# Kernel tuning notes

Hardware: AMD Instinct MI355X
Metric: run time of the kernel (lower is better)

The kernel has to match this reference:

```python
import jax, jax.numpy as jnp
import numpy as np

D_MODEL = 1024
D_FF = 1024
NUM_EXPERTS = 8
TOP_K = 2


def setup_inputs() -> dict:
    key = jax.random.key(0)
    ks = jax.random.split(key, 5)
    s_in = 1.0 / np.sqrt(D_MODEL)
    s_ff = 1.0 / np.sqrt(D_FF)
    return {
        "x": jax.random.normal(ks[0], (4, 2048, D_MODEL), dtype=jnp.float32),
        "gate_w": jax.random.normal(ks[1], (NUM_EXPERTS, D_MODEL), dtype=jnp.float32) * s_in,
        # torch Linear weight layout: [out_features, in_features], stacked over experts
        "w_gate": jax.random.normal(ks[2], (NUM_EXPERTS, D_FF, D_MODEL), dtype=jnp.float32) * s_in,
        "w_up": jax.random.normal(ks[3], (NUM_EXPERTS, D_FF, D_MODEL), dtype=jnp.float32) * s_in,
        "w_down": jax.random.normal(ks[4], (NUM_EXPERTS, D_MODEL, D_FF), dtype=jnp.float32) * s_ff,
    }


def reference(x, gate_w, w_gate, w_up, w_down):
    B, S, D = x.shape
    T = B * S
    E = gate_w.shape[0]
    xt = x.reshape(T, D)

    # Router
    logits = xt @ gate_w.T                      # [T, E]
    probs = jax.nn.softmax(logits, axis=-1)
    top_v, top_i = jax.lax.top_k(probs, TOP_K)  # [T, K]
    top_v = top_v / jnp.sum(top_v, axis=-1, keepdims=True)

    tokens_per_expert = jnp.sum(jax.nn.one_hot(top_i, E, dtype=jnp.float32), axis=(0, 1))  # [E]
    f = tokens_per_expert / jnp.sum(tokens_per_expert)
    P = jnp.mean(probs, axis=0)
    aux_loss = E * jnp.sum(f * P)

    # Combine weights: per-token weight for each expert (sum over top-k slots)
    combine = jnp.zeros((T, E), dtype=x.dtype).at[jnp.arange(T)[:, None], top_i].add(top_v)  # [T, E]

    # Dense per-expert SwiGLU (equivalent math to masked gather/scatter loop)
    g = jnp.einsum('td,efd->etf', xt, w_gate)   # [E, T, F]
    u = jnp.einsum('td,efd->etf', xt, w_up)     # [E, T, F]
    act = jax.nn.silu(g) * u
    eo = jnp.einsum('etf,edf->etd', act, w_down)  # [E, T, D]

    out = jnp.einsum('te,etd->td', combine, eo).reshape(B, S, D)
    return out, aux_loss, tokens_per_expert
```

## Files before the change

### kernel.cpp

```cpp
#include <hip/hip_runtime.h>


#define T_TOK   8192
#define DM      1024
#define DFF     1024
#define NE      8
#define TOTS    (2 * T_TOK)
#define R1_BLK  2048
#define CVT_BLK 2048

typedef __attribute__((ext_vector_type(8))) short bf16x8;
typedef __attribute__((ext_vector_type(4))) float f32x4;

#define ASYNC16(gp, lp) __builtin_amdgcn_global_load_lds( \
    (const __attribute__((address_space(1))) unsigned int*)(gp), \
    (__attribute__((address_space(3))) unsigned int*)(lp), 16, 0, 0)

__device__ __forceinline__ unsigned short f2bf(float f) {
    union { float f; unsigned u; } c; c.f = f;
    unsigned r = c.u + 0x7fffu + ((c.u >> 16) & 1u);
    return (unsigned short)(r >> 16);
}
__device__ __forceinline__ float bf2f(unsigned short h) {
    union { unsigned u; float f; } c; c.u = ((unsigned)h) << 16;
    return c.f;
}

__global__ __launch_bounds__(256) void pre_kernel(
    const float* __restrict__ x, const float* __restrict__ gate_w,
    const float* __restrict__ s0, const float* __restrict__ s1, const float* __restrict__ s2,
    unsigned short* __restrict__ d0, unsigned short* __restrict__ d1, unsigned short* __restrict__ d2,
    unsigned short* __restrict__ xb,
    int* __restrict__ topi, float2* __restrict__ topw, float* __restrict__ psum_part)
{
    int tid = threadIdx.x;
    int sub = blockIdx.x >> 1;

    if (blockIdx.x & 1) {
        int base = sub * 256 + tid;
        #pragma unroll
        for (int it = 0; it < 12; ++it) {
            int idx = base + it * (CVT_BLK * 256);
            int seg = idx >> 21;
            int off = (idx & ((1 << 21) - 1)) * 4;
            const float* s = (seg == 0) ? s0 : (seg == 1) ? s1 : s2;
            unsigned short* d = (seg == 0) ? d0 : (seg == 1) ? d1 : d2;
            float4 v = *(const float4*)(s + off);
            ushort4 o;
            o.x = f2bf(v.x); o.y = f2bf(v.y); o.z = f2bf(v.z); o.w = f2bf(v.w);
            *(ushort4*)(d + off) = o;
        }
        return;
    }

    __shared__ float gw[NE * DM];
    __shared__ float blk_psum[NE];

    for (int i = tid; i < NE * DM; i += 256) gw[i] = gate_w[i];
    if (tid < NE) blk_psum[tid] = 0.f;
    __syncthreads();

    int wv = tid >> 6, lane = tid & 63;
    int t = sub * 4 + wv;

    float acc[NE];
    #pragma unroll
    for (int e = 0; e < NE; ++e) acc[e] = 0.f;
    const float* xr = x + (size_t)t * DM;
    unsigned short* xbr = xb + (size_t)t * DM;
    #pragma unroll 4
    for (int i = 0; i < DM / 64; ++i) {
        float xv = xr[i * 64 + lane];
        xbr[i * 64 + lane] = f2bf(xv);
        #pragma unroll
        for (int e = 0; e < NE; ++e)
            acc[e] += xv * gw[e * DM + i * 64 + lane];
    }
    #pragma unroll
    for (int e = 0; e < NE; ++e) {
        float v = acc[e];
        #pragma unroll
        for (int s = 32; s > 0; s >>= 1) v += __shfl_xor(v, s, 64);
        acc[e] = v;
    }
    if (lane == 0) {
        float mx = acc[0];
        #pragma unroll
        for (int e = 1; e < NE; ++e) mx = fmaxf(mx, acc[e]);
        float p[NE], sum = 0.f;
        #pragma unroll
        for (int e = 0; e < NE; ++e) { p[e] = expf(acc[e] - mx); sum += p[e]; }
        float inv = 1.f / sum;
        #pragma unroll
        for (int e = 0; e < NE; ++e) { p[e] *= inv; atomicAdd(&blk_psum[e], p[e]); }
        int i1 = 0; float v1 = p[0];
        #pragma unroll
        for (int e = 1; e < NE; ++e) if (p[e] > v1) { v1 = p[e]; i1 = e; }
        int i2 = -1; float v2 = -1.f;
        #pragma unroll
        for (int e = 0; e < NE; ++e) { if (e == i1) continue; if (p[e] > v2) { v2 = p[e]; i2 = e; } }
        float winv = 1.f / (v1 + v2);
        topi[t] = i1 | (i2 << 8);
        topw[t] = make_float2(v1 * winv, v2 * winv);
    }
    __syncthreads();
    if (tid < NE) psum_part[sub * NE + tid] = blk_psum[tid];
}

__global__ __launch_bounds__(1024) void scatfin_kernel(
    const int* __restrict__ topi, const float* __restrict__ psum_part,
    int* __restrict__ elist, int2* __restrict__ cidx,
    int* __restrict__ ecnt, int* __restrict__ ebaseg, float* __restrict__ out_tail)
{
    __shared__ int lcnt[NE], run[NE], cb[NE], ebase[NE];
    __shared__ float parts[NE];
    __shared__ float red[1024];
    int tid = threadIdx.x;

    if (tid < NE) run[tid] = 0;
    __syncthreads();
    #pragma unroll
    for (int ch = 0; ch < T_TOK / 1024; ++ch) {
        int tt = ch * 1024 + tid;
        int pk = topi[tt];
        int e1 = pk & 0xff, e2 = (pk >> 8) & 0xff;
        if (tid < NE) lcnt[tid] = 0;
        __syncthreads();
        int p1 = atomicAdd(&lcnt[e1], 1);
        int p2 = atomicAdd(&lcnt[e2], 1);
        __syncthreads();
        if (tid < NE) { cb[tid] = run[tid]; run[tid] += lcnt[tid]; }
        __syncthreads();
        cidx[tt] = make_int2(cb[e1] + p1, cb[e2] + p2);
    }
    __syncthreads();
    if (tid == 0) {
        int s = 0;
        for (int e = 0; e < NE; ++e) { ebase[e] = s; s += run[e]; }
    }
    __syncthreads();
    #pragma unroll
    for (int ch = 0; ch < T_TOK / 1024; ++ch) {
        int tt = ch * 1024 + tid;
        int pk = topi[tt];
        int e1 = pk & 0xff, e2 = (pk >> 8) & 0xff;
        int2 pp = cidx[tt];
        int r1 = ebase[e1] + pp.x, r2 = ebase[e2] + pp.y;
        elist[r1] = tt;
        elist[r2] = tt;
        cidx[tt] = make_int2(r1, r2);
    }
    if (tid < NE) { ecnt[tid] = run[tid]; ebaseg[tid] = ebase[tid]; }

    int e = tid & 7, b0 = tid >> 3;
    float s = 0.f;
    for (int b = b0; b < R1_BLK; b += 128) s += psum_part[b * NE + e];
    red[tid] = s;
    __syncthreads();
    if (tid < NE) {
        float tot = 0.f;
        #pragma unroll
        for (int j = 0; j < 128; ++j) tot += red[tid + NE * j];
        float P = tot / (float)T_TOK;
        float f = (float)run[tid] / (float)(2 * T_TOK);
        parts[tid] = f * P;
        out_tail[1 + tid] = (float)run[tid];
    }
    __syncthreads();
    if (tid == 0) {
        float s2 = 0.f;
        for (int i = 0; i < NE; ++i) s2 += parts[i];
        out_tail[0] = (float)NE * s2;
    }
}

__global__ __launch_bounds__(256) void gemm1_kernel(
    const unsigned short* __restrict__ xb,
    const unsigned short* __restrict__ wgb,
    const unsigned short* __restrict__ wub,
    const int* __restrict__ elist, const int* __restrict__ ecnt,
    const int* __restrict__ ebaseg,
    unsigned short* __restrict__ Hbuf)
{
    int e = blockIdx.z, mt = blockIdx.y, ft = blockIdx.x;
    int ne = ecnt[e];
    if (mt * 128 >= ne) return;
    int base = ebaseg[e];

    __shared__ unsigned short As[128 * 64];
    __shared__ unsigned short Gs[64 * 64];
    __shared__ unsigned short Us[64 * 64];
    __shared__ int tok[128];

    int tid = threadIdx.x;
    if (tid < 128) {
        int slot = base + mt * 128 + tid;
        tok[tid] = elist[min(slot, TOTS - 1)];
    }
    __syncthreads();

    int wave = tid >> 6, lane = tid & 63;
    int quad = lane >> 4, col = lane & 15;
    int cr = tid >> 3;
    int cl = ((tid & 7) ^ (cr & 7)) * 8;

    const size_t woff = (size_t)e * (size_t)DFF * DM;
    const unsigned short* ap[4];
    #pragma unroll
    for (int j = 0; j < 4; ++j) ap[j] = xb + (size_t)tok[j * 32 + cr] * DM + cl;
    const unsigned short* gp[2];
    const unsigned short* up[2];
    #pragma unroll
    for (int j = 0; j < 2; ++j) {
        gp[j] = wgb + woff + (size_t)(ft * 64 + j * 32 + cr) * DM + cl;
        up[j] = wub + woff + (size_t)(ft * 64 + j * 32 + cr) * DM + cl;
    }
    unsigned short* lA = As + wave * 512;
    unsigned short* lG = Gs + wave * 512;
    unsigned short* lU = Us + wave * 512;

    f32x4 accG[2][4], accU[2][4];
    #pragma unroll
    for (int i = 0; i < 2; ++i)
        #pragma unroll
        for (int n = 0; n < 4; ++n) { accG[i][n] = (f32x4){0,0,0,0}; accU[i][n] = (f32x4){0,0,0,0}; }

    for (int k0 = 0; k0 < DM; k0 += 64) {
        __syncthreads();
        #pragma unroll
        for (int j = 0; j < 4; ++j) ASYNC16(ap[j] + k0, lA + j * 2048);
        #pragma unroll
        for (int j = 0; j < 2; ++j) {
            ASYNC16(gp[j] + k0, lG + j * 2048);
            ASYNC16(up[j] + k0, lU + j * 2048);
        }
        __syncthreads();
        #pragma unroll
        for (int ksoff = 0; ksoff < 8; ksoff += 4) {
            bf16x8 a[2], g[4], u[4];
            #pragma unroll
            for (int i = 0; i < 2; ++i) {
                int m = wave * 32 + i * 16 + col;
                a[i] = *(const bf16x8*)&As[m * 64 + ((quad + ksoff) ^ (m & 7)) * 8];
            }
            #pragma unroll
            for (int n = 0; n < 4; ++n) {
                int nb = n * 16 + col;
                int off = nb * 64 + ((quad + ksoff) ^ (nb & 7)) * 8;
                g[n] = *(const bf16x8*)&Gs[off];
                u[n] = *(const bf16x8*)&Us[off];
            }
            #pragma unroll
            for (int i = 0; i < 2; ++i)
                #pragma unroll
                for (int n = 0; n < 4; ++n) {
                    accG[i][n] = __builtin_amdgcn_mfma_f32_16x16x32_bf16(a[i], g[n], accG[i][n], 0, 0, 0);
                    accU[i][n] = __builtin_amdgcn_mfma_f32_16x16x32_bf16(a[i], u[n], accU[i][n], 0, 0, 0);
                }
        }
    }
    #pragma unroll
    for (int i = 0; i < 2; ++i) {
        #pragma unroll
        for (int r = 0; r < 4; ++r) {
            int pos = mt * 128 + wave * 32 + i * 16 + quad * 4 + r;
            if (pos >= ne) continue;
            unsigned short* hr = Hbuf + (size_t)(base + pos) * DFF + ft * 64 + col;
            #pragma unroll
            for (int n = 0; n < 4; ++n) {
                float gg = accG[i][n][r], uu = accU[i][n][r];
                float h = (gg / (1.f + expf(-gg))) * uu;
                hr[n * 16] = f2bf(h);
            }
        }
    }
}

__global__ __launch_bounds__(256) void gemm2_kernel(
    const unsigned short* __restrict__ Hbuf,
    const unsigned short* __restrict__ wdb,
    const int* __restrict__ ecnt, const int* __restrict__ ebaseg,
    unsigned short* __restrict__ eo)
{
    int e = blockIdx.z, mt = blockIdx.y, dt = blockIdx.x;
    int ne = ecnt[e];
    if (mt * 128 >= ne) return;
    int base = ebaseg[e];

    __shared__ unsigned short As[128 * 64];
    __shared__ unsigned short Bs[128 * 64];

    int tid = threadIdx.x;
    int wave = tid >> 6, lane = tid & 63;
    int quad = lane >> 4, col = lane & 15;
    int wr = (wave >> 1) * 64, wc = (wave & 1) * 64;
    int cr = tid >> 3;
    int cl = ((tid & 7) ^ (cr & 7)) * 8;

    const size_t woff = (size_t)e * (size_t)DM * DFF;
    const unsigned short* ap[4];
    const unsigned short* bp[4];
    #pragma unroll
    for (int j = 0; j < 4; ++j) {
        int hrow = min(base + mt * 128 + j * 32 + cr, TOTS - 1);
        ap[j] = Hbuf + (size_t)hrow * DFF + cl;
        bp[j] = wdb + woff + (size_t)(dt * 128 + j * 32 + cr) * DFF + cl;
    }
    unsigned short* lA = As + wave * 512;
    unsigned short* lB = Bs + wave * 512;

    f32x4 acc[4][4];
    #pragma unroll
    for (int i = 0; i < 4; ++i)
        #pragma unroll
        for (int n = 0; n < 4; ++n) acc[i][n] = (f32x4){0,0,0,0};

    for (int k0 = 0; k0 < DFF; k0 += 64) {
        __syncthreads();
        #pragma unroll
        for (int j = 0; j < 4; ++j) {
            ASYNC16(ap[j] + k0, lA + j * 2048);
            ASYNC16(bp[j] + k0, lB + j * 2048);
        }
        __syncthreads();
        #pragma unroll
        for (int ksoff = 0; ksoff < 8; ksoff += 4) {
            bf16x8 a[4], b[4];
            #pragma unroll
            for (int i = 0; i < 4; ++i) {
                int m = wr + i * 16 + col;
                a[i] = *(const bf16x8*)&As[m * 64 + ((quad + ksoff) ^ (m & 7)) * 8];
            }
            #pragma unroll
            for (int n = 0; n < 4; ++n) {
                int nb = wc + n * 16 + col;
                b[n] = *(const bf16x8*)&Bs[nb * 64 + ((quad + ksoff) ^ (nb & 7)) * 8];
            }
            #pragma unroll
            for (int i = 0; i < 4; ++i)
                #pragma unroll
                for (int n = 0; n < 4; ++n)
                    acc[i][n] = __builtin_amdgcn_mfma_f32_16x16x32_bf16(a[i], b[n], acc[i][n], 0, 0, 0);
        }
    }
    #pragma unroll
    for (int i = 0; i < 4; ++i) {
        #pragma unroll
        for (int r = 0; r < 4; ++r) {
            int pos = mt * 128 + wr + i * 16 + quad * 4 + r;
            if (pos >= ne) continue;
            unsigned short* er = eo + (size_t)(base + pos) * DM + dt * 128 + wc + col;
            #pragma unroll
            for (int n = 0; n < 4; ++n)
                er[n * 16] = f2bf(acc[i][n][r]);
        }
    }
}

__global__ __launch_bounds__(256) void combine_kernel(
    const unsigned short* __restrict__ eo, const float2* __restrict__ topw,
    const int2* __restrict__ cidx, float* __restrict__ out)
{
    int idx = blockIdx.x * 256 + threadIdx.x;
    int t = idx >> 7;
    int c = (idx & 127) << 3;
    float2 w = topw[t];
    int2 rr = cidx[t];
    const unsigned short* p0 = eo + (size_t)rr.x * DM + c;
    const unsigned short* p1 = eo + (size_t)rr.y * DM + c;
    ushort4 a0 = *(const ushort4*)p0;
    ushort4 a1 = *(const ushort4*)(p0 + 4);
    ushort4 b0 = *(const ushort4*)p1;
    ushort4 b1 = *(const ushort4*)(p1 + 4);
    float* orow = out + (size_t)t * DM + c;
    float4 o0, o1;
    o0.x = w.x * bf2f(a0.x) + w.y * bf2f(b0.x);
    o0.y = w.x * bf2f(a0.y) + w.y * bf2f(b0.y);
    o0.z = w.x * bf2f(a0.z) + w.y * bf2f(b0.z);
    o0.w = w.x * bf2f(a0.w) + w.y * bf2f(b0.w);
    o1.x = w.x * bf2f(a1.x) + w.y * bf2f(b1.x);
    o1.y = w.x * bf2f(a1.y) + w.y * bf2f(b1.y);
    o1.z = w.x * bf2f(a1.z) + w.y * bf2f(b1.z);
    o1.w = w.x * bf2f(a1.w) + w.y * bf2f(b1.w);
    *(float4*)orow = o0;
    *(float4*)(orow + 4) = o1;
}

extern "C" void kernel_launch(void* const* d_in, const int* in_sizes, int n_in,
                              void* d_out, int out_size, void* d_ws, size_t ws_size,
                              hipStream_t stream) {
    const float* x      = (const float*)d_in[0];
    const float* gate_w = (const float*)d_in[1];
    const float* w_gate = (const float*)d_in[2];
    const float* w_up   = (const float*)d_in[3];
    const float* w_down = (const float*)d_in[4];
    float* out = (float*)d_out;

    char* p = (char*)d_ws;
    unsigned short* xb   = (unsigned short*)p; p += (size_t)T_TOK * DM * 2;
    unsigned short* wgb  = (unsigned short*)p; p += (size_t)NE * DFF * DM * 2;
    unsigned short* wub  = (unsigned short*)p; p += (size_t)NE * DFF * DM * 2;
    unsigned short* wdb  = (unsigned short*)p; p += (size_t)NE * DM * DFF * 2;
    unsigned short* Hbuf = (unsigned short*)p; p += (size_t)TOTS * DFF * 2;
    int*   elist = (int*)p;   p += (size_t)TOTS * 4;
    int*   ecnt  = (int*)p;   p += NE * 4;
    int*   ebaseg= (int*)p;   p += NE * 4;
    int*   topi  = (int*)p;   p += (size_t)T_TOK * 4;
    float2* topw = (float2*)p; p += (size_t)T_TOK * 8;
    int2*  cidx  = (int2*)p;  p += (size_t)T_TOK * 8;
    float* psum_part = (float*)p; p += (size_t)R1_BLK * NE * 4;
    unsigned short* eo = wgb;

    pre_kernel<<<R1_BLK + CVT_BLK, 256, 0, stream>>>(
        x, gate_w, w_gate, w_up, w_down, wgb, wub, wdb,
        xb, topi, topw, psum_part);
    scatfin_kernel<<<1, 1024, 0, stream>>>(topi, psum_part, elist, cidx, ecnt, ebaseg,
                                           out + (size_t)T_TOK * DM);
    gemm1_kernel<<<dim3(DFF / 64, TOTS / 128, NE), 256, 0, stream>>>(
        xb, wgb, wub, elist, ecnt, ebaseg, Hbuf);
    gemm2_kernel<<<dim3(DM / 128, TOTS / 128, NE), 256, 0, stream>>>(
        Hbuf, wdb, ecnt, ebaseg, eo);
    combine_kernel<<<T_TOK * DM / 8 / 256, 256, 0, stream>>>(eo, topw, cidx, out);
}
```

Baseline: 340.0 us.

## Rewrite expert GEMMs with 256x256 tiles, double-buffered LDS and interleaved async loads

Both grouped expert GEMMs move to 512-thread blocks with 256-row by 256-column output tiles. LDS is double-buffered so the next K slice loads through async global-to-LDS copies while MFMAs run on the current one, with explicit barriers, vmcnt waits and setprio around the MFMA bursts. The larger tiles raise data reuse per block and the pipeline is meant to hide load latency. In exchange each block uses 128KB of LDS, which limits occupancy, the grid has fewer blocks so load balance across experts gets coarser, and the hand-placed waitcnt/barrier sequencing is fragile.

```diff
diff --git a/kernel.cpp b/kernel.cpp
--- a/kernel.cpp
+++ b/kernel.cpp
@@ -15,6 +15,10 @@
 #define ASYNC16(gp, lp) __builtin_amdgcn_global_load_lds( \
     (const __attribute__((address_space(1))) unsigned int*)(gp), \
     (__attribute__((address_space(3))) unsigned int*)(lp), 16, 0, 0)
+
+#define BAR()   __builtin_amdgcn_s_barrier()
+#define SFENCE() __builtin_amdgcn_sched_barrier(0)
+#define VMCNT2() asm volatile("s_waitcnt vmcnt(2)" ::: "memory")
 
 __device__ __forceinline__ unsigned short f2bf(float f) {
     union { float f; unsigned u; } c; c.f = f;
@@ -174,7 +178,7 @@
     }
 }
 
-__global__ __launch_bounds__(256) void gemm1_kernel(
+__global__ __launch_bounds__(512, 2) void gemm1_kernel(
     const unsigned short* __restrict__ xb,
     const unsigned short* __restrict__ wgb,
     const unsigned short* __restrict__ wub,
@@ -184,88 +188,149 @@
 {
     int e = blockIdx.z, mt = blockIdx.y, ft = blockIdx.x;
     int ne = ecnt[e];
-    if (mt * 128 >= ne) return;
+    if (mt * 256 >= ne) return;
     int base = ebaseg[e];
 
-    __shared__ unsigned short As[128 * 64];
-    __shared__ unsigned short Gs[64 * 64];
-    __shared__ unsigned short Us[64 * 64];
-    __shared__ int tok[128];
+    __shared__ unsigned short As[2][256 * 64];
+    __shared__ unsigned short Bs[2][256 * 64];
+    __shared__ int tok[256];
 
     int tid = threadIdx.x;
-    if (tid < 128) {
-        int slot = base + mt * 128 + tid;
-        tok[tid] = elist[min(slot, TOTS - 1)];
-    }
+    if (tid < 256) tok[tid] = elist[min(base + mt * 256 + tid, TOTS - 1)];
     __syncthreads();
 
     int wave = tid >> 6, lane = tid & 63;
+    int wq = wave >> 1, wn = wave & 1;
     int quad = lane >> 4, col = lane & 15;
     int cr = tid >> 3;
     int cl = ((tid & 7) ^ (cr & 7)) * 8;
 
     const size_t woff = (size_t)e * (size_t)DFF * DM;
     const unsigned short* ap[4];
-    #pragma unroll
-    for (int j = 0; j < 4; ++j) ap[j] = xb + (size_t)tok[j * 32 + cr] * DM + cl;
-    const unsigned short* gp[2];
-    const unsigned short* up[2];
+    const unsigned short* bp[4];
+    #pragma unroll
+    for (int j = 0; j < 4; ++j)
+        ap[j] = xb + (size_t)tok[j * 64 + cr] * DM + cl;
     #pragma unroll
     for (int j = 0; j < 2; ++j) {
-        gp[j] = wgb + woff + (size_t)(ft * 64 + j * 32 + cr) * DM + cl;
-        up[j] = wub + woff + (size_t)(ft * 64 + j * 32 + cr) * DM + cl;
-    }
-    unsigned short* lA = As + wave * 512;
-    unsigned short* lG = Gs + wave * 512;
-    unsigned short* lU = Us + wave * 512;
-
-    f32x4 accG[2][4], accU[2][4];
-    #pragma unroll
-    for (int i = 0; i < 2; ++i)
+        bp[j]     = wgb + woff + (size_t)(ft * 128 + j * 64 + cr) * DM + cl;
+        bp[j + 2] = wub + woff + (size_t)(ft * 128 + j * 64 + cr) * DM + cl;
+    }
+
+    f32x4 accG[4][4], accU[4][4];
+    #pragma unroll
+    for (int i = 0; i < 4; ++i)
         #pragma unroll
         for (int n = 0; n < 4; ++n) { accG[i][n] = (f32x4){0,0,0,0}; accU[i][n] = (f32x4){0,0,0,0}; }
 
-    for (int k0 = 0; k0 < DM; k0 += 64) {
-        __syncthreads();
-        #pragma unroll
-        for (int j = 0; j < 4; ++j) ASYNC16(ap[j] + k0, lA + j * 2048);
-        #pragma unroll
-        for (int j = 0; j < 2; ++j) {
-            ASYNC16(gp[j] + k0, lG + j * 2048);
-            ASYNC16(up[j] + k0, lU + j * 2048);
-        }
-        __syncthreads();
-        #pragma unroll
-        for (int ksoff = 0; ksoff < 8; ksoff += 4) {
-            bf16x8 a[2], g[4], u[4];
-            #pragma unroll
-            for (int i = 0; i < 2; ++i) {
-                int m = wave * 32 + i * 16 + col;
-                a[i] = *(const bf16x8*)&As[m * 64 + ((quad + ksoff) ^ (m & 7)) * 8];
-            }
-            #pragma unroll
-            for (int n = 0; n < 4; ++n) {
-                int nb = n * 16 + col;
-                int off = nb * 64 + ((quad + ksoff) ^ (nb & 7)) * 8;
-                g[n] = *(const bf16x8*)&Gs[off];
-                u[n] = *(const bf16x8*)&Us[off];
-            }
-            #pragma unroll
-            for (int i = 0; i < 2; ++i)
-                #pragma unroll
-                for (int n = 0; n < 4; ++n) {
-                    accG[i][n] = __builtin_amdgcn_mfma_f32_16x16x32_bf16(a[i], g[n], accG[i][n], 0, 0, 0);
-                    accU[i][n] = __builtin_amdgcn_mfma_f32_16x16x32_bf16(a[i], u[n], accU[i][n], 0, 0, 0);
-                }
-        }
-    }
-    #pragma unroll
-    for (int i = 0; i < 2; ++i) {
+    {
+        unsigned short* A0 = &As[0][wave * 512];
+        unsigned short* B0 = &Bs[0][wave * 512];
+        #pragma unroll
+        for (int j = 0; j < 4; ++j) ASYNC16(ap[j], A0 + j * 4096);
+        #pragma unroll
+        for (int j = 0; j < 4; ++j) ASYNC16(bp[j], B0 + j * 4096);
+    }
+    asm volatile("s_waitcnt vmcnt(0)" ::: "memory");
+    BAR(); SFENCE();
+
+    for (int t = 0; t < 16; ++t) {
+        int cur = t & 1;
+        int ks = (t < 15 ? (t + 1) : 15) * 64;
+        unsigned short* An = &As[cur ^ 1][wave * 512];
+        unsigned short* Bn = &Bs[cur ^ 1][wave * 512];
+        const unsigned short* Ac = &As[cur][0];
+        const unsigned short* Bc = &Bs[cur][0];
+
+        bf16x8 a[4], b[4];
+        #pragma unroll
+        for (int i = 0; i < 4; ++i) {
+            int m = wq * 64 + i * 16 + col;
+            a[i] = *(const bf16x8*)&Ac[m * 64 + (quad ^ (m & 7)) * 8];
+        }
+        #pragma unroll
+        for (int n = 0; n < 4; ++n) {
+            int nb = wn * 64 + n * 16 + col;
+            b[n] = *(const bf16x8*)&Bc[nb * 64 + (quad ^ (nb & 7)) * 8];
+        }
+        ASYNC16(ap[0] + ks, An);
+        ASYNC16(ap[1] + ks, An + 4096);
+        VMCNT2();
+        BAR(); SFENCE();
+        __builtin_amdgcn_s_setprio(1);
+        #pragma unroll
+        for (int i = 0; i < 4; ++i)
+            #pragma unroll
+            for (int n = 0; n < 4; ++n)
+                accG[i][n] = __builtin_amdgcn_mfma_f32_16x16x32_bf16(a[i], b[n], accG[i][n], 0, 0, 0);
+        __builtin_amdgcn_s_setprio(0);
+        BAR(); SFENCE();
+
+        #pragma unroll
+        for (int n = 0; n < 4; ++n) {
+            int nb = 128 + wn * 64 + n * 16 + col;
+            b[n] = *(const bf16x8*)&Bc[nb * 64 + (quad ^ (nb & 7)) * 8];
+        }
+        ASYNC16(ap[2] + ks, An + 8192);
+        ASYNC16(ap[3] + ks, An + 12288);
+        BAR(); SFENCE();
+        __builtin_amdgcn_s_setprio(1);
+        #pragma unroll
+        for (int i = 0; i < 4; ++i)
+            #pragma unroll
+            for (int n = 0; n < 4; ++n)
+                accU[i][n] = __builtin_amdgcn_mfma_f32_16x16x32_bf16(a[i], b[n], accU[i][n], 0, 0, 0);
+        __builtin_amdgcn_s_setprio(0);
+        BAR(); SFENCE();
+
+        #pragma unroll
+        for (int i = 0; i < 4; ++i) {
+            int m = wq * 64 + i * 16 + col;
+            a[i] = *(const bf16x8*)&Ac[m * 64 + ((quad + 4) ^ (m & 7)) * 8];
+        }
+        #pragma unroll
+        for (int n = 0; n < 4; ++n) {
+            int nb = wn * 64 + n * 16 + col;
+            b[n] = *(const bf16x8*)&Bc[nb * 64 + ((quad + 4) ^ (nb & 7)) * 8];
+        }
+        ASYNC16(bp[0] + ks, Bn);
+        ASYNC16(bp[1] + ks, Bn + 4096);
+        BAR(); SFENCE();
+        __builtin_amdgcn_s_setprio(1);
+        #pragma unroll
+        for (int i = 0; i < 4; ++i)
+            #pragma unroll
+            for (int n = 0; n < 4; ++n)
+                accG[i][n] = __builtin_amdgcn_mfma_f32_16x16x32_bf16(a[i], b[n], accG[i][n], 0, 0, 0);
+        __builtin_amdgcn_s_setprio(0);
+        BAR(); SFENCE();
+
+        #pragma unroll
+        for (int n = 0; n < 4; ++n) {
+            int nb = 128 + wn * 64 + n * 16 + col;
+            b[n] = *(const bf16x8*)&Bc[nb * 64 + ((quad + 4) ^ (nb & 7)) * 8];
+        }
+        ASYNC16(bp[2] + ks, Bn + 8192);
+        ASYNC16(bp[3] + ks, Bn + 12288);
+        VMCNT2();
+        BAR(); SFENCE();
+        __builtin_amdgcn_s_setprio(1);
+        #pragma unroll
+        for (int i = 0; i < 4; ++i)
+            #pragma unroll
+            for (int n = 0; n < 4; ++n)
+                accU[i][n] = __builtin_amdgcn_mfma_f32_16x16x32_bf16(a[i], b[n], accU[i][n], 0, 0, 0);
+        __builtin_amdgcn_s_setprio(0);
+        BAR(); SFENCE();
+    }
+
+    #pragma unroll
+    for (int i = 0; i < 4; ++i) {
         #pragma unroll
         for (int r = 0; r < 4; ++r) {
-            int pos = mt * 128 + wave * 32 + i * 16 + quad * 4 + r;
+            int pos = mt * 256 + wq * 64 + i * 16 + quad * 4 + r;
             if (pos >= ne) continue;
-            unsigned short* hr = Hbuf + (size_t)(base + pos) * DFF + ft * 64 + col;
+            unsigned short* hr = Hbuf + (size_t)(base + pos) * DFF + ft * 128 + wn * 64 + col;
             #pragma unroll
             for (int n = 0; n < 4; ++n) {
                 float gg = accG[i][n][r], uu = accU[i][n][r];
@@ -276,7 +341,7 @@
     }
 }
 
-__global__ __launch_bounds__(256) void gemm2_kernel(
+__global__ __launch_bounds__(512, 2) void gemm2_kernel(
     const unsigned short* __restrict__ Hbuf,
     const unsigned short* __restrict__ wdb,
     const int* __restrict__ ecnt, const int* __restrict__ ebaseg,
@@ -284,16 +349,16 @@
 {
     int e = blockIdx.z, mt = blockIdx.y, dt = blockIdx.x;
     int ne = ecnt[e];
-    if (mt * 128 >= ne) return;
+    if (mt * 256 >= ne) return;
     int base = ebaseg[e];
 
-    __shared__ unsigned short As[128 * 64];
-    __shared__ unsigned short Bs[128 * 64];
+    __shared__ unsigned short As[2][256 * 64];
+    __shared__ unsigned short Bs[2][256 * 64];
 
     int tid = threadIdx.x;
     int wave = tid >> 6, lane = tid & 63;
+    int wq = wave >> 1, wn = wave & 1;
     int quad = lane >> 4, col = lane & 15;
-    int wr = (wave >> 1) * 64, wc = (wave & 1) * 64;
     int cr = tid >> 3;
     int cl = ((tid & 7) ^ (cr & 7)) * 8;
 
@@ -302,57 +367,128 @@
     const unsigned short* bp[4];
     #pragma unroll
     for (int j = 0; j < 4; ++j) {
-        int hrow = min(base + mt * 128 + j * 32 + cr, TOTS - 1);
+        int hrow = min(base + mt * 256 + j * 64 + cr, TOTS - 1);
         ap[j] = Hbuf + (size_t)hrow * DFF + cl;
-        bp[j] = wdb + woff + (size_t)(dt * 128 + j * 32 + cr) * DFF + cl;
-    }
-    unsigned short* lA = As + wave * 512;
-    unsigned short* lB = Bs + wave * 512;
-
-    f32x4 acc[4][4];
+        bp[j] = wdb + woff + (size_t)(dt * 256 + j * 64 + cr) * DFF + cl;
+    }
+
+    f32x4 acc[4][8];
     #pragma unroll
     for (int i = 0; i < 4; ++i)
         #pragma unroll
-        for (int n = 0; n < 4; ++n) acc[i][n] = (f32x4){0,0,0,0};
-
-    for (int k0 = 0; k0 < DFF; k0 += 64) {
-        __syncthreads();
-        #pragma unroll
-        for (int j = 0; j < 4; ++j) {
-            ASYNC16(ap[j] + k0, lA + j * 2048);
-            ASYNC16(bp[j] + k0, lB + j * 2048);
-        }
-        __syncthreads();
-        #pragma unroll
-        for (int ksoff = 0; ksoff < 8; ksoff += 4) {
-            bf16x8 a[4], b[4];
-            #pragma unroll
-            for (int i = 0; i < 4; ++i) {
-                int m = wr + i * 16 + col;
-                a[i] = *(const bf16x8*)&As[m * 64 + ((quad + ksoff) ^ (m & 7)) * 8];
-            }
-            #pragma unroll
-            for (int n = 0; n < 4; ++n) {
-                int nb = wc + n * 16 + col;
-                b[n] = *(const bf16x8*)&Bs[nb * 64 + ((quad + ksoff) ^ (nb & 7)) * 8];
-            }
-            #pragma unroll
-            for (int i = 0; i < 4; ++i)
-                #pragma unroll
-                for (int n = 0; n < 4; ++n)
-                    acc[i][n] = __builtin_amdgcn_mfma_f32_16x16x32_bf16(a[i], b[n], acc[i][n], 0, 0, 0);
-        }
-    }
+        for (int n = 0; n < 8; ++n) acc[i][n] = (f32x4){0,0,0,0};
+
+    {
+        unsigned short* A0 = &As[0][wave * 512];
+        unsigned short* B0 = &Bs[0][wave * 512];
+        #pragma unroll
+        for (int j = 0; j < 4; ++j) ASYNC16(ap[j], A0 + j * 4096);
+        #pragma unroll
+        for (int j = 0; j < 4; ++j) ASYNC16(bp[j], B0 + j * 4096);
+    }
+    asm volatile("s_waitcnt vmcnt(0)" ::: "memory");
+    BAR(); SFENCE();
+
+    for (int t = 0; t < 16; ++t) {
+        int cur = t & 1;
+        int ks = (t < 15 ? (t + 1) : 15) * 64;
+        unsigned short* An = &As[cur ^ 1][wave * 512];
+        unsigned short* Bn = &Bs[cur ^ 1][wave * 512];
+        const unsigned short* Ac = &As[cur][0];
+        const unsigned short* Bc = &Bs[cur][0];
+
+        bf16x8 a[4], b[4];
+        #pragma unroll
+        for (int i = 0; i < 4; ++i) {
+            int m = wq * 64 + i * 16 + col;
+            a[i] = *(const bf16x8*)&Ac[m * 64 + (quad ^ (m & 7)) * 8];
+        }
+        #pragma unroll
+        for (int n = 0; n < 4; ++n) {
+            int nb = n * 32 + wn * 16 + col;
+            b[n] = *(const bf16x8*)&Bc[nb * 64 + (quad ^ (nb & 7)) * 8];
+        }
+        ASYNC16(ap[0] + ks, An);
+        ASYNC16(ap[1] + ks, An + 4096);
+        VMCNT2();
+        BAR(); SFENCE();
+        __builtin_amdgcn_s_setprio(1);
+        #pragma unroll
+        for (int i = 0; i < 4; ++i)
+            #pragma unroll
+            for (int n = 0; n < 4; ++n)
+                acc[i][n] = __builtin_amdgcn_mfma_f32_16x16x32_bf16(a[i], b[n], acc[i][n], 0, 0, 0);
+        __builtin_amdgcn_s_setprio(0);
+        BAR(); SFENCE();
+
+        #pragma unroll
+        for (int n = 0; n < 4; ++n) {
+            int nb = 128 + n * 32 + wn * 16 + col;
+            b[n] = *(const bf16x8*)&Bc[nb * 64 + (quad ^ (nb & 7)) * 8];
+        }
+        ASYNC16(ap[2] + ks, An + 8192);
+        ASYNC16(ap[3] + ks, An + 12288);
+        BAR(); SFENCE();
+        __builtin_amdgcn_s_setprio(1);
+        #pragma unroll
+        for (int i = 0; i < 4; ++i)
+            #pragma unroll
+            for (int n = 0; n < 4; ++n)
+                acc[i][n + 4] = __builtin_amdgcn_mfma_f32_16x16x32_bf16(a[i], b[n], acc[i][n + 4], 0, 0, 0);
+        __builtin_amdgcn_s_setprio(0);
+        BAR(); SFENCE();
+
+        #pragma unroll
+        for (int i = 0; i < 4; ++i) {
+            int m = wq * 64 + i * 16 + col;
+            a[i] = *(const bf16x8*)&Ac[m * 64 + ((quad + 4) ^ (m & 7)) * 8];
+        }
+        #pragma unroll
+        for (int n = 0; n < 4; ++n) {
+            int nb = n * 32 + wn * 16 + col;
+            b[n] = *(const bf16x8*)&Bc[nb * 64 + ((quad + 4) ^ (nb & 7)) * 8];
+        }
+        ASYNC16(bp[0] + ks, Bn);
+        ASYNC16(bp[1] + ks, Bn + 4096);
+        BAR(); SFENCE();
+        __builtin_amdgcn_s_setprio(1);
+        #pragma unroll
+        for (int i = 0; i < 4; ++i)
+            #pragma unroll
+            for (int n = 0; n < 4; ++n)
+                acc[i][n] = __builtin_amdgcn_mfma_f32_16x16x32_bf16(a[i], b[n], acc[i][n], 0, 0, 0);
+        __builtin_amdgcn_s_setprio(0);
+        BAR(); SFENCE();
+
+        #pragma unroll
+        for (int n = 0; n < 4; ++n) {
+            int nb = 128 + n * 32 + wn * 16 + col;
+            b[n] = *(const bf16x8*)&Bc[nb * 64 + ((quad + 4) ^ (nb & 7)) * 8];
+        }
+        ASYNC16(bp[2] + ks, Bn + 8192);
+        ASYNC16(bp[3] + ks, Bn + 12288);
+        VMCNT2();
+        BAR(); SFENCE();
+        __builtin_amdgcn_s_setprio(1);
+        #pragma unroll
+        for (int i = 0; i < 4; ++i)
+            #pragma unroll
+            for (int n = 0; n < 4; ++n)
+                acc[i][n + 4] = __builtin_amdgcn_mfma_f32_16x16x32_bf16(a[i], b[n], acc[i][n + 4], 0, 0, 0);
+        __builtin_amdgcn_s_setprio(0);
+        BAR(); SFENCE();
+    }
+
     #pragma unroll
     for (int i = 0; i < 4; ++i) {
         #pragma unroll
         for (int r = 0; r < 4; ++r) {
-            int pos = mt * 128 + wr + i * 16 + quad * 4 + r;
+            int pos = mt * 256 + wq * 64 + i * 16 + quad * 4 + r;
             if (pos >= ne) continue;
-            unsigned short* er = eo + (size_t)(base + pos) * DM + dt * 128 + wc + col;
-            #pragma unroll
-            for (int n = 0; n < 4; ++n)
-                er[n * 16] = f2bf(acc[i][n][r]);
+            unsigned short* er = eo + (size_t)(base + pos) * DM + dt * 256 + wn * 16 + col;
+            #pragma unroll
+            for (int n = 0; n < 8; ++n)
+                er[n * 32] = f2bf(acc[i][n][r]);
         }
     }
 }
@@ -416,9 +552,9 @@
         xb, topi, topw, psum_part);
     scatfin_kernel<<<1, 1024, 0, stream>>>(topi, psum_part, elist, cidx, ecnt, ebaseg,
                                            out + (size_t)T_TOK * DM);
-    gemm1_kernel<<<dim3(DFF / 64, TOTS / 128, NE), 256, 0, stream>>>(
+    gemm1_kernel<<<dim3(DFF / 128, TOTS / 256, NE), 512, 0, stream>>>(
         xb, wgb, wub, elist, ecnt, ebaseg, Hbuf);
-    gemm2_kernel<<<dim3(DM / 128, TOTS / 128, NE), 256, 0, stream>>>(
+    gemm2_kernel<<<dim3(DM / 256, TOTS / 256, NE), 512, 0, stream>>>(
         Hbuf, wdb, ecnt, ebaseg, eo);
     combine_kernel<<<T_TOK * DM / 8 / 256, 256, 0, stream>>>(eo, topw, cidx, out);
 }
```

New measurement: 355.9 us. +4.7%, slower.

## Use 32x32x16 MFMA and 256-row M tiles in both expert GEMMs

Applied to the files above, without the earlier changes.

Both grouped GEMM kernels double the token tile from 128 to 256 rows and switch from 16x16x32 to 32x32x16 bf16 MFMA instructions, reorganizing the wave layout to 2x2 with 128-row halves. Each weight tile loaded to LDS is now reused across twice as many tokens, and the larger MFMA shape needs fewer LDS fragment reads per flop. The cost is more LDS per block and more accumulator registers, which may lower occupancy. Fewer blocks are launched, and with about 2048 tokens per expert the last tile may be less full, which could leave CUs idle.

```diff
diff --git a/kernel.cpp b/kernel.cpp
--- a/kernel.cpp
+++ b/kernel.cpp
@@ -11,6 +11,7 @@
 
 typedef __attribute__((ext_vector_type(8))) short bf16x8;
 typedef __attribute__((ext_vector_type(4))) float f32x4;
+typedef __attribute__((ext_vector_type(16))) float f32x16;
 
 #define ASYNC16(gp, lp) __builtin_amdgcn_global_load_lds( \
     (const __attribute__((address_space(1))) unsigned int*)(gp), \
@@ -184,30 +185,29 @@
 {
     int e = blockIdx.z, mt = blockIdx.y, ft = blockIdx.x;
     int ne = ecnt[e];
-    if (mt * 128 >= ne) return;
+    if (mt * 256 >= ne) return;
     int base = ebaseg[e];
 
-    __shared__ unsigned short As[128 * 64];
+    __shared__ unsigned short As[256 * 64];
     __shared__ unsigned short Gs[64 * 64];
     __shared__ unsigned short Us[64 * 64];
-    __shared__ int tok[128];
+    __shared__ int tok[256];
 
     int tid = threadIdx.x;
-    if (tid < 128) {
-        int slot = base + mt * 128 + tid;
-        tok[tid] = elist[min(slot, TOTS - 1)];
-    }
+    tok[tid] = elist[min(base + mt * 256 + tid, TOTS - 1)];
     __syncthreads();
 
     int wave = tid >> 6, lane = tid & 63;
-    int quad = lane >> 4, col = lane & 15;
+    int wm = wave >> 1, wn = wave & 1;
+    int h = lane >> 5, l31 = lane & 31;
     int cr = tid >> 3;
     int cl = ((tid & 7) ^ (cr & 7)) * 8;
 
     const size_t woff = (size_t)e * (size_t)DFF * DM;
-    const unsigned short* ap[4];
-    #pragma unroll
-    for (int j = 0; j < 4; ++j) ap[j] = xb + (size_t)tok[j * 32 + cr] * DM + cl;
+    const unsigned short* ap[8];
+    #pragma unroll
+    for (int j = 0; j < 8; ++j)
+        ap[j] = xb + (size_t)tok[j * 32 + cr] * DM + cl;
     const unsigned short* gp[2];
     const unsigned short* up[2];
     #pragma unroll
@@ -219,16 +219,17 @@
     unsigned short* lG = Gs + wave * 512;
     unsigned short* lU = Us + wave * 512;
 
-    f32x4 accG[2][4], accU[2][4];
-    #pragma unroll
-    for (int i = 0; i < 2; ++i)
-        #pragma unroll
-        for (int n = 0; n < 4; ++n) { accG[i][n] = (f32x4){0,0,0,0}; accU[i][n] = (f32x4){0,0,0,0}; }
+    f32x16 accG[4], accU[4];
+    #pragma unroll
+    for (int i = 0; i < 4; ++i) {
+        accG[i] = (f32x16){0,0,0,0,0,0,0,0,0,0,0,0,0,0,0,0};
+        accU[i] = (f32x16){0,0,0,0,0,0,0,0,0,0,0,0,0,0,0,0};
+    }
 
     for (int k0 = 0; k0 < DM; k0 += 64) {
         __syncthreads();
         #pragma unroll
-        for (int j = 0; j < 4; ++j) ASYNC16(ap[j] + k0, lA + j * 2048);
+        for (int j = 0; j < 8; ++j) ASYNC16(ap[j] + k0, lA + j * 2048);
         #pragma unroll
         for (int j = 0; j < 2; ++j) {
             ASYNC16(gp[j] + k0, lG + j * 2048);
@@ -236,42 +237,33 @@
         }
         __syncthreads();
         #pragma unroll
-        for (int ksoff = 0; ksoff < 8; ksoff += 4) {
-            bf16x8 a[2], g[4], u[4];
+        for (int ks = 0; ks < 4; ++ks) {
+            int col8 = ks * 2 + h;
+            bf16x8 a[4], g, u;
             #pragma unroll
-            for (int i = 0; i < 2; ++i) {
-                int m = wave * 32 + i * 16 + col;
-                a[i] = *(const bf16x8*)&As[m * 64 + ((quad + ksoff) ^ (m & 7)) * 8];
+            for (int i = 0; i < 4; ++i) {
+                int m = wm * 128 + i * 32 + l31;
+                a[i] = *(const bf16x8*)&As[m * 64 + (col8 ^ (m & 7)) * 8];
             }
+            int gc = wn * 32 + l31;
+            g = *(const bf16x8*)&Gs[gc * 64 + (col8 ^ (gc & 7)) * 8];
+            u = *(const bf16x8*)&Us[gc * 64 + (col8 ^ (gc & 7)) * 8];
             #pragma unroll
-            for (int n = 0; n < 4; ++n) {
-                int nb = n * 16 + col;
-                int off = nb * 64 + ((quad + ksoff) ^ (nb & 7)) * 8;
-                g[n] = *(const bf16x8*)&Gs[off];
-                u[n] = *(const bf16x8*)&Us[off];
+            for (int i = 0; i < 4; ++i) {
+                accG[i] = __builtin_amdgcn_mfma_f32_32x32x16_bf16(a[i], g, accG[i], 0, 0, 0);
+                accU[i] = __builtin_amdgcn_mfma_f32_32x32x16_bf16(a[i], u, accU[i], 0, 0, 0);
             }
-            #pragma unroll
-            for (int i = 0; i < 2; ++i)
-                #pragma unroll
-                for (int n = 0; n < 4; ++n) {
-                    accG[i][n] = __builtin_amdgcn_mfma_f32_16x16x32_bf16(a[i], g[n], accG[i][n], 0, 0, 0);
-                    accU[i][n] = __builtin_amdgcn_mfma_f32_16x16x32_bf16(a[i], u[n], accU[i][n], 0, 0, 0);
-                }
-        }
-    }
-    #pragma unroll
-    for (int i = 0; i < 2; ++i) {
-        #pragma unroll
-        for (int r = 0; r < 4; ++r) {
-            int pos = mt * 128 + wave * 32 + i * 16 + quad * 4 + r;
+        }
+    }
+    #pragma unroll
+    for (int i = 0; i < 4; ++i) {
+        #pragma unroll
+        for (int r = 0; r < 16; ++r) {
+            int pos = mt * 256 + wm * 128 + i * 32 + 4 * h + (r & 3) + 8 * (r >> 2);
             if (pos >= ne) continue;
-            unsigned short* hr = Hbuf + (size_t)(base + pos) * DFF + ft * 64 + col;
-            #pragma unroll
-            for (int n = 0; n < 4; ++n) {
-                float gg = accG[i][n][r], uu = accU[i][n][r];
-                float h = (gg / (1.f + expf(-gg))) * uu;
-                hr[n * 16] = f2bf(h);
-            }
+            float gg = accG[i][r], uu = accU[i][r];
+            float hv = (gg / (1.f + expf(-gg))) * uu;
+            Hbuf[(size_t)(base + pos) * DFF + ft * 64 + wn * 32 + l31] = f2bf(hv);
         }
     }
 }
@@ -284,75 +276,78 @@
 {
     int e = blockIdx.z, mt = blockIdx.y, dt = blockIdx.x;
     int ne = ecnt[e];
-    if (mt * 128 >= ne) return;
+    if (mt * 256 >= ne) return;
     int base = ebaseg[e];
 
-    __shared__ unsigned short As[128 * 64];
+    __shared__ unsigned short As[256 * 64];
     __shared__ unsigned short Bs[128 * 64];
 
     int tid = threadIdx.x;
     int wave = tid >> 6, lane = tid & 63;
-    int quad = lane >> 4, col = lane & 15;
-    int wr = (wave >> 1) * 64, wc = (wave & 1) * 64;
+    int wm = wave >> 1, wn = wave & 1;
+    int h = lane >> 5, l31 = lane & 31;
     int cr = tid >> 3;
     int cl = ((tid & 7) ^ (cr & 7)) * 8;
 
     const size_t woff = (size_t)e * (size_t)DM * DFF;
-    const unsigned short* ap[4];
+    const unsigned short* ap[8];
     const unsigned short* bp[4];
     #pragma unroll
-    for (int j = 0; j < 4; ++j) {
-        int hrow = min(base + mt * 128 + j * 32 + cr, TOTS - 1);
+    for (int j = 0; j < 8; ++j) {
+        int hrow = min(base + mt * 256 + j * 32 + cr, TOTS - 1);
         ap[j] = Hbuf + (size_t)hrow * DFF + cl;
+    }
+    #pragma unroll
+    for (int j = 0; j < 4; ++j)
         bp[j] = wdb + woff + (size_t)(dt * 128 + j * 32 + cr) * DFF + cl;
-    }
+
     unsigned short* lA = As + wave * 512;
     unsigned short* lB = Bs + wave * 512;
 
-    f32x4 acc[4][4];
+    f32x16 acc[4][2];
     #pragma unroll
     for (int i = 0; i < 4; ++i)
         #pragma unroll
-        for (int n = 0; n < 4; ++n) acc[i][n] = (f32x4){0,0,0,0};
+        for (int n = 0; n < 2; ++n)
+            acc[i][n] = (f32x16){0,0,0,0,0,0,0,0,0,0,0,0,0,0,0,0};
 
     for (int k0 = 0; k0 < DFF; k0 += 64) {
         __syncthreads();
         #pragma unroll
-        for (int j = 0; j < 4; ++j) {
-            ASYNC16(ap[j] + k0, lA + j * 2048);
-            ASYNC16(bp[j] + k0, lB + j * 2048);
-        }
-        __syncthreads();
-        #pragma unroll
-        for (int ksoff = 0; ksoff < 8; ksoff += 4) {
-            bf16x8 a[4], b[4];
+        for (int j = 0; j < 8; ++j) ASYNC16(ap[j] + k0, lA + j * 2048);
+        #pragma unroll
+        for (int j = 0; j < 4; ++j) ASYNC16(bp[j] + k0, lB + j * 2048);
+        __syncthreads();
+        #pragma unroll
+        for (int ks = 0; ks < 4; ++ks) {
+            int col8 = ks * 2 + h;
+            bf16x8 a[4], b[2];
             #pragma unroll
             for (int i = 0; i < 4; ++i) {
-                int m = wr + i * 16 + col;
-                a[i] = *(const bf16x8*)&As[m * 64 + ((quad + ksoff) ^ (m & 7)) * 8];
+                int m = wm * 128 + i * 32 + l31;
+                a[i] = *(const bf16x8*)&As[m * 64 + (col8 ^ (m & 7)) * 8];
             }
             #pragma unroll
-            for (int n = 0; n < 4; ++n) {
-                int nb = wc + n * 16 + col;
-                b[n] = *(const bf16x8*)&Bs[nb * 64 + ((quad + ksoff) ^ (nb & 7)) * 8];
+            for (int n = 0; n < 2; ++n) {
+                int bc = wn * 64 + n * 32 + l31;
+                b[n] = *(const bf16x8*)&Bs[bc * 64 + (col8 ^ (bc & 7)) * 8];
             }
             #pragma unroll
             for (int i = 0; i < 4; ++i)
                 #pragma unroll
-                for (int n = 0; n < 4; ++n)
-                    acc[i][n] = __builtin_amdgcn_mfma_f32_16x16x32_bf16(a[i], b[n], acc[i][n], 0, 0, 0);
+                for (int n = 0; n < 2; ++n)
+                    acc[i][n] = __builtin_amdgcn_mfma_f32_32x32x16_bf16(a[i], b[n], acc[i][n], 0, 0, 0);
         }
     }
     #pragma unroll
     for (int i = 0; i < 4; ++i) {
         #pragma unroll
-        for (int r = 0; r < 4; ++r) {
-            int pos = mt * 128 + wr + i * 16 + quad * 4 + r;
+        for (int r = 0; r < 16; ++r) {
+            int pos = mt * 256 + wm * 128 + i * 32 + 4 * h + (r & 3) + 8 * (r >> 2);
             if (pos >= ne) continue;
-            unsigned short* er = eo + (size_t)(base + pos) * DM + dt * 128 + wc + col;
-            #pragma unroll
-            for (int n = 0; n < 4; ++n)
-                er[n * 16] = f2bf(acc[i][n][r]);
+            unsigned short* er = eo + (size_t)(base + pos) * DM + dt * 128 + wn * 64 + l31;
+            er[0]  = f2bf(acc[i][0][r]);
+            er[32] = f2bf(acc[i][1][r]);
         }
     }
 }
@@ -416,9 +411,9 @@
         xb, topi, topw, psum_part);
     scatfin_kernel<<<1, 1024, 0, stream>>>(topi, psum_part, elist, cidx, ecnt, ebaseg,
                                            out + (size_t)T_TOK * DM);
-    gemm1_kernel<<<dim3(DFF / 64, TOTS / 128, NE), 256, 0, stream>>>(
+    gemm1_kernel<<<dim3(DFF / 64, TOTS / 256, NE), 256, 0, stream>>>(
         xb, wgb, wub, elist, ecnt, ebaseg, Hbuf);
-    gemm2_kernel<<<dim3(DM / 128, TOTS / 128, NE), 256, 0, stream>>>(
+    gemm2_kernel<<<dim3(DM / 128, TOTS / 256, NE), 256, 0, stream>>>(
         Hbuf, wdb, ecnt, ebaseg, eo);
     combine_kernel<<<T_TOK * DM / 8 / 256, 256, 0, stream>>>(eo, topw, cidx, out);
 }
```

Result: slower. 437.9 us (+28.8%).

## Double M-tile to 256 rows in both expert GEMMs for more reuse

Applied to the files above, without the earlier changes.

Both grouped GEMM kernels now process 256 token rows per block instead of 128. Each wave computes a 64-row strip, with 4x4 accumulators for each of gate and up in gemm1 and 4x8 in gemm2. The aim is to cut weight-tile reloads per output and raise MFMA work per LDS load. The cost is a doubled accumulator register footprint, more LDS per block (hence launch_bounds(256,2)), fewer blocks in flight, and more padding waste when the last tile of an expert is partly empty.

```diff
diff --git a/kernel.cpp b/kernel.cpp
--- a/kernel.cpp
+++ b/kernel.cpp
@@ -174,7 +174,7 @@
     }
 }
 
-__global__ __launch_bounds__(256) void gemm1_kernel(
+__global__ __launch_bounds__(256, 2) void gemm1_kernel(
     const unsigned short* __restrict__ xb,
     const unsigned short* __restrict__ wgb,
     const unsigned short* __restrict__ wub,
@@ -184,19 +184,16 @@
 {
     int e = blockIdx.z, mt = blockIdx.y, ft = blockIdx.x;
     int ne = ecnt[e];
-    if (mt * 128 >= ne) return;
+    if (mt * 256 >= ne) return;
     int base = ebaseg[e];
 
-    __shared__ unsigned short As[128 * 64];
+    __shared__ unsigned short As[256 * 64];
     __shared__ unsigned short Gs[64 * 64];
     __shared__ unsigned short Us[64 * 64];
-    __shared__ int tok[128];
+    __shared__ int tok[256];
 
     int tid = threadIdx.x;
-    if (tid < 128) {
-        int slot = base + mt * 128 + tid;
-        tok[tid] = elist[min(slot, TOTS - 1)];
-    }
+    tok[tid] = elist[min(base + mt * 256 + tid, TOTS - 1)];
     __syncthreads();
 
     int wave = tid >> 6, lane = tid & 63;
@@ -205,9 +202,10 @@
     int cl = ((tid & 7) ^ (cr & 7)) * 8;
 
     const size_t woff = (size_t)e * (size_t)DFF * DM;
-    const unsigned short* ap[4];
-    #pragma unroll
-    for (int j = 0; j < 4; ++j) ap[j] = xb + (size_t)tok[j * 32 + cr] * DM + cl;
+    const unsigned short* ap[8];
+    #pragma unroll
+    for (int j = 0; j < 8; ++j)
+        ap[j] = xb + (size_t)tok[j * 32 + cr] * DM + cl;
     const unsigned short* gp[2];
     const unsigned short* up[2];
     #pragma unroll
@@ -219,16 +217,16 @@
     unsigned short* lG = Gs + wave * 512;
     unsigned short* lU = Us + wave * 512;
 
-    f32x4 accG[2][4], accU[2][4];
-    #pragma unroll
-    for (int i = 0; i < 2; ++i)
+    f32x4 accG[4][4], accU[4][4];
+    #pragma unroll
+    for (int i = 0; i < 4; ++i)
         #pragma unroll
         for (int n = 0; n < 4; ++n) { accG[i][n] = (f32x4){0,0,0,0}; accU[i][n] = (f32x4){0,0,0,0}; }
 
     for (int k0 = 0; k0 < DM; k0 += 64) {
         __syncthreads();
         #pragma unroll
-        for (int j = 0; j < 4; ++j) ASYNC16(ap[j] + k0, lA + j * 2048);
+        for (int j = 0; j < 8; ++j) ASYNC16(ap[j] + k0, lA + j * 2048);
         #pragma unroll
         for (int j = 0; j < 2; ++j) {
             ASYNC16(gp[j] + k0, lG + j * 2048);
@@ -237,10 +235,10 @@
         __syncthreads();
         #pragma unroll
         for (int ksoff = 0; ksoff < 8; ksoff += 4) {
-            bf16x8 a[2], g[4], u[4];
-            #pragma unroll
-            for (int i = 0; i < 2; ++i) {
-                int m = wave * 32 + i * 16 + col;
+            bf16x8 a[4], g[4], u[4];
+            #pragma unroll
+            for (int i = 0; i < 4; ++i) {
+                int m = wave * 64 + i * 16 + col;
                 a[i] = *(const bf16x8*)&As[m * 64 + ((quad + ksoff) ^ (m & 7)) * 8];
             }
             #pragma unroll
@@ -251,7 +249,7 @@
                 u[n] = *(const bf16x8*)&Us[off];
             }
             #pragma unroll
-            for (int i = 0; i < 2; ++i)
+            for (int i = 0; i < 4; ++i)
                 #pragma unroll
                 for (int n = 0; n < 4; ++n) {
                     accG[i][n] = __builtin_amdgcn_mfma_f32_16x16x32_bf16(a[i], g[n], accG[i][n], 0, 0, 0);
@@ -260,10 +258,10 @@
         }
     }
     #pragma unroll
-    for (int i = 0; i < 2; ++i) {
+    for (int i = 0; i < 4; ++i) {
         #pragma unroll
         for (int r = 0; r < 4; ++r) {
-            int pos = mt * 128 + wave * 32 + i * 16 + quad * 4 + r;
+            int pos = mt * 256 + wave * 64 + i * 16 + quad * 4 + r;
             if (pos >= ne) continue;
             unsigned short* hr = Hbuf + (size_t)(base + pos) * DFF + ft * 64 + col;
             #pragma unroll
@@ -276,7 +274,7 @@
     }
 }
 
-__global__ __launch_bounds__(256) void gemm2_kernel(
+__global__ __launch_bounds__(256, 2) void gemm2_kernel(
     const unsigned short* __restrict__ Hbuf,
     const unsigned short* __restrict__ wdb,
     const int* __restrict__ ecnt, const int* __restrict__ ebaseg,
@@ -284,62 +282,63 @@
 {
     int e = blockIdx.z, mt = blockIdx.y, dt = blockIdx.x;
     int ne = ecnt[e];
-    if (mt * 128 >= ne) return;
+    if (mt * 256 >= ne) return;
     int base = ebaseg[e];
 
-    __shared__ unsigned short As[128 * 64];
+    __shared__ unsigned short As[256 * 64];
     __shared__ unsigned short Bs[128 * 64];
 
     int tid = threadIdx.x;
     int wave = tid >> 6, lane = tid & 63;
     int quad = lane >> 4, col = lane & 15;
-    int wr = (wave >> 1) * 64, wc = (wave & 1) * 64;
     int cr = tid >> 3;
     int cl = ((tid & 7) ^ (cr & 7)) * 8;
 
     const size_t woff = (size_t)e * (size_t)DM * DFF;
-    const unsigned short* ap[4];
+    const unsigned short* ap[8];
     const unsigned short* bp[4];
     #pragma unroll
-    for (int j = 0; j < 4; ++j) {
-        int hrow = min(base + mt * 128 + j * 32 + cr, TOTS - 1);
+    for (int j = 0; j < 8; ++j) {
+        int hrow = min(base + mt * 256 + j * 32 + cr, TOTS - 1);
         ap[j] = Hbuf + (size_t)hrow * DFF + cl;
+    }
+    #pragma unroll
+    for (int j = 0; j < 4; ++j)
         bp[j] = wdb + woff + (size_t)(dt * 128 + j * 32 + cr) * DFF + cl;
-    }
+
     unsigned short* lA = As + wave * 512;
     unsigned short* lB = Bs + wave * 512;
 
-    f32x4 acc[4][4];
+    f32x4 acc[4][8];
     #pragma unroll
     for (int i = 0; i < 4; ++i)
         #pragma unroll
-        for (int n = 0; n < 4; ++n) acc[i][n] = (f32x4){0,0,0,0};
+        for (int n = 0; n < 8; ++n) acc[i][n] = (f32x4){0,0,0,0};
 
     for (int k0 = 0; k0 < DFF; k0 += 64) {
         __syncthreads();
         #pragma unroll
-        for (int j = 0; j < 4; ++j) {
-            ASYNC16(ap[j] + k0, lA + j * 2048);
-            ASYNC16(bp[j] + k0, lB + j * 2048);
-        }
+        for (int j = 0; j < 8; ++j) ASYNC16(ap[j] + k0, lA + j * 2048);
+        #pragma unroll
+        for (int j = 0; j < 4; ++j) ASYNC16(bp[j] + k0, lB + j * 2048);
         __syncthreads();
         #pragma unroll
         for (int ksoff = 0; ksoff < 8; ksoff += 4) {
-            bf16x8 a[4], b[4];
+            bf16x8 a[4], b[8];
             #pragma unroll
             for (int i = 0; i < 4; ++i) {
-                int m = wr + i * 16 + col;
+                int m = wave * 64 + i * 16 + col;
                 a[i] = *(const bf16x8*)&As[m * 64 + ((quad + ksoff) ^ (m & 7)) * 8];
             }
             #pragma unroll
-            for (int n = 0; n < 4; ++n) {
-                int nb = wc + n * 16 + col;
+            for (int n = 0; n < 8; ++n) {
+                int nb = n * 16 + col;
                 b[n] = *(const bf16x8*)&Bs[nb * 64 + ((quad + ksoff) ^ (nb & 7)) * 8];
             }
             #pragma unroll
             for (int i = 0; i < 4; ++i)
                 #pragma unroll
-                for (int n = 0; n < 4; ++n)
+                for (int n = 0; n < 8; ++n)
                     acc[i][n] = __builtin_amdgcn_mfma_f32_16x16x32_bf16(a[i], b[n], acc[i][n], 0, 0, 0);
         }
     }
@@ -347,11 +346,11 @@
     for (int i = 0; i < 4; ++i) {
         #pragma unroll
         for (int r = 0; r < 4; ++r) {
-            int pos = mt * 128 + wr + i * 16 + quad * 4 + r;
+            int pos = mt * 256 + wave * 64 + i * 16 + quad * 4 + r;
             if (pos >= ne) continue;
-            unsigned short* er = eo + (size_t)(base + pos) * DM + dt * 128 + wc + col;
-            #pragma unroll
-            for (int n = 0; n < 4; ++n)
+            unsigned short* er = eo + (size_t)(base + pos) * DM + dt * 128 + col;
+            #pragma unroll
+            for (int n = 0; n < 8; ++n)
                 er[n * 16] = f2bf(acc[i][n][r]);
         }
     }
@@ -416,9 +415,9 @@
         xb, topi, topw, psum_part);
     scatfin_kernel<<<1, 1024, 0, stream>>>(topi, psum_part, elist, cidx, ecnt, ebaseg,
                                            out + (size_t)T_TOK * DM);
-    gemm1_kernel<<<dim3(DFF / 64, TOTS / 128, NE), 256, 0, stream>>>(
+    gemm1_kernel<<<dim3(DFF / 64, TOTS / 256, NE), 256, 0, stream>>>(
         xb, wgb, wub, elist, ecnt, ebaseg, Hbuf);
-    gemm2_kernel<<<dim3(DM / 128, TOTS / 128, NE), 256, 0, stream>>>(
+    gemm2_kernel<<<dim3(DM / 128, TOTS / 256, NE), 256, 0, stream>>>(
         Hbuf, wdb, ecnt, ebaseg, eo);
     combine_kernel<<<T_TOK * DM / 8 / 256, 256, 0, stream>>>(eo, topw, cidx, out);
 }
```

Result: slower. 347.5 us (+2.2%).
